# Performance work log

Hardware: AMD Instinct MI355X
Metric: run time of the kernel (lower is better)

Reference implementation:

```python
import jax, jax.numpy as jnp
import numpy as np
from jax import lax

B, C, H, W = 2, 128, 128, 128
Hs, Ws = 64, 64
DG, KK = 8, 9          # deformable groups, kernel positions (3x3)
CG = C // DG           # channels per deformable group = 16
COUT = C // 2          # dcn output channels = 64


def setup_inputs() -> dict:
    key = jax.random.key(0)
    ks = jax.random.split(key, 9)
    s = 0.05
    return {
        "feat_l": jax.random.normal(ks[0], (B, C, H, W), jnp.float32),
        "feat_s": jax.random.normal(ks[1], (B, C, Hs, Ws), jnp.float32),
        "fsm_w": jax.random.normal(ks[2], (C, C, 1, 1), jnp.float32) * s,
        "offset_w": jax.random.normal(ks[3], (C, 2 * C, 1, 1), jnp.float32) * s,
        "com_w": jax.random.normal(ks[4], (3 * DG * KK, C, 3, 3), jnp.float32) * s,
        "com_b": jax.random.normal(ks[5], (3 * DG * KK,), jnp.float32) * s,
        "dcn_w": jax.random.normal(ks[6], (COUT, C, 3, 3), jnp.float32) * s,
        "dcn_b": jax.random.normal(ks[7], (COUT,), jnp.float32) * s,
        "cat_w": jax.random.normal(ks[8], (C, COUT, 1, 1), jnp.float32) * s,
    }


def _conv(x, w, pad):
    return lax.conv_general_dilated(x, w, (1, 1), [(pad, pad), (pad, pad)],
                                    dimension_numbers=("NCHW", "OIHW", "NCHW"))


def _bilinear(feat_g, py, px):
    # feat_g: [B,DG,CG,H,W]; py/px: [B,DG,KK,H,W] fractional sample coords.
    Hf, Wf = feat_g.shape[-2], feat_g.shape[-1]
    y0 = jnp.floor(py)
    x0 = jnp.floor(px)
    ly = py - y0
    lx = px - x0
    y0i = y0.astype(jnp.int32)
    x0i = x0.astype(jnp.int32)
    flat = feat_g.reshape(B, DG, 1, CG, Hf * Wf)  # broadcast over KK

    def gather(yi, xi, wgt):
        valid = ((yi >= 0) & (yi < Hf) & (xi >= 0) & (xi < Wf)).astype(feat_g.dtype)
        idx = (jnp.clip(yi, 0, Hf - 1) * Wf + jnp.clip(xi, 0, Wf - 1))
        idx = idx.reshape(B, DG, KK, 1, H * W)
        v = jnp.take_along_axis(flat, idx, axis=-1)  # [B,DG,KK,CG,H*W]
        return v * (wgt * valid).reshape(B, DG, KK, 1, H * W)

    acc = (gather(y0i, x0i, (1 - ly) * (1 - lx))
           + gather(y0i, x0i + 1, (1 - ly) * lx)
           + gather(y0i + 1, x0i, ly * (1 - lx))
           + gather(y0i + 1, x0i + 1, ly * lx))
    return acc.reshape(B, DG, KK, CG, H, W)


def reference(feat_l, feat_s, fsm_w, offset_w, com_w, com_b, dcn_w, dcn_b, cat_w):
    # nearest-neighbor upsample of feat_s to feat_l's HxW (F.interpolate nearest)
    idx_h = (jnp.arange(H) * Hs) // H
    idx_w = (jnp.arange(W) * Ws) // W
    feat_up = feat_s[:, :, idx_h][:, :, :, idx_w]

    feat_arm = jax.nn.relu(_conv(feat_l, fsm_w, 0))                       # FSM (1x1 conv+relu)
    off_feat = jax.nn.relu(_conv(jnp.concatenate([feat_arm, feat_up * 2], axis=1), offset_w, 0))

    # DCNv2 pack: 3x3 conv -> (o1, o2, mask)
    om = _conv(off_feat, com_w, 1) + com_b[None, :, None, None]
    o1, o2, m = jnp.split(om, 3, axis=1)
    offset = jnp.concatenate([o1, o2], axis=1).reshape(B, DG, KK, 2, H, W)  # (y,x) per (g,pos)
    mask = jax.nn.sigmoid(m).reshape(B, DG, KK, H, W)

    # sampling coords: p + kernel offset + learned offset (stride=1, pad=1, dil=1)
    kyy = (jnp.arange(KK) // 3 - 1).astype(jnp.float32)
    kxx = (jnp.arange(KK) % 3 - 1).astype(jnp.float32)
    py = (jnp.arange(H, dtype=jnp.float32)[None, None, None, :, None]
          + kyy[None, None, :, None, None] + offset[:, :, :, 0])
    px = (jnp.arange(W, dtype=jnp.float32)[None, None, None, None, :]
          + kxx[None, None, :, None, None] + offset[:, :, :, 1])

    feat_g = feat_up.reshape(B, DG, CG, H, W)
    val = _bilinear(feat_g, py, px) * mask[:, :, :, None]  # [B,DG,KK,CG,H,W]

    w_r = dcn_w.reshape(COUT, DG, CG, KK)
    out = jnp.einsum('bgkchw,ogck->bohw', val, w_r) + dcn_b[None, :, None, None]
    feat_align = jax.nn.relu(out)

    return jax.nn.relu(_conv(feat_align, cat_w, 0)) + feat_arm
```

## Files before the change

### kernel.cpp

```cpp
#include <hip/hip_runtime.h>
#include <cstdint>
#include <cstddef>


typedef _Float16 f16x8 __attribute__((ext_vector_type(8)));
typedef _Float16 f16x4 __attribute__((ext_vector_type(4)));
typedef float    f32x4 __attribute__((ext_vector_type(4)));

__device__ __forceinline__ float relu_(float x) { return fmaxf(x, 0.f); }

template<int MODE, int CIN>
__global__ __launch_bounds__(256) void conv1x1_kernel(
    const float* __restrict__ in1, const float* __restrict__ in2,
    const float* __restrict__ Wm, float* __restrict__ out)
{
  constexpr int IN1C = (MODE == 2) ? 64 : 128;
  const int b  = blockIdx.y;
  const int p0 = blockIdx.x * 64;
  const int tid = threadIdx.x;
  const int tx = tid & 7;
  const int ty = tid >> 3;

  __shared__ float Xs[16][64];
  __shared__ float Wt[16][128];

  float acc[4][8];
#pragma unroll
  for (int i = 0; i < 4; ++i)
#pragma unroll
    for (int j = 0; j < 8; ++j) acc[i][j] = 0.f;

  const int cS  = tid >> 4;
  const int pxS = (tid & 15) * 4;
  const int ocS = (tid & 15) * 8;

  for (int cc = 0; cc < CIN; cc += 16) {
    __syncthreads();
    {
      int gc = cc + cS;
      float4 v;
      if (MODE == 1 && gc >= 128) {
        int sc = gc - 128;
        float t[4];
#pragma unroll
        for (int j = 0; j < 4; ++j) {
          int pp = p0 + pxS + j;
          int hh = pp >> 7, ww = pp & 127;
          t[j] = 2.f * in2[((size_t)(b * 128 + sc) << 12) + ((hh >> 1) << 6) + (ww >> 1)];
        }
        v = make_float4(t[0], t[1], t[2], t[3]);
      } else {
        v = *(const float4*)(in1 + ((size_t)(b * IN1C + gc) << 14) + p0 + pxS);
      }
      *(float4*)&Xs[cS][pxS] = v;
#pragma unroll
      for (int j = 0; j < 8; ++j)
        Wt[cS][ocS + j] = Wm[(ocS + j) * CIN + cc + cS];
    }
    __syncthreads();
#pragma unroll
    for (int c = 0; c < 16; ++c) {
      float4 wv = *(const float4*)&Wt[c][ty * 4];
      float4 x0 = *(const float4*)&Xs[c][tx * 8];
      float4 x1 = *(const float4*)&Xs[c][tx * 8 + 4];
      float xs[8] = {x0.x, x0.y, x0.z, x0.w, x1.x, x1.y, x1.z, x1.w};
      float wf[4] = {wv.x, wv.y, wv.z, wv.w};
#pragma unroll
      for (int i = 0; i < 4; ++i)
#pragma unroll
        for (int j = 0; j < 8; ++j)
          acc[i][j] = fmaf(wf[i], xs[j], acc[i][j]);
    }
  }

#pragma unroll
  for (int i = 0; i < 4; ++i) {
    int oc = ty * 4 + i;
    size_t base = ((size_t)(b * 128 + oc) << 14) + p0 + tx * 8;
    float r[8];
#pragma unroll
    for (int j = 0; j < 8; ++j) r[j] = relu_(acc[i][j]);
    if (MODE == 2) {
#pragma unroll
      for (int j = 0; j < 8; ++j) r[j] += in2[base + j];
    }
    *(float4*)(out + base)     = make_float4(r[0], r[1], r[2], r[3]);
    *(float4*)(out + base + 4) = make_float4(r[4], r[5], r[6], r[7]);
  }
}

__global__ __launch_bounds__(256) void t2h2_kernel(
    const float* __restrict__ fl, const float* __restrict__ fs,
    _Float16* __restrict__ flTh, _Float16* __restrict__ fsTh)
{
  const int bx = blockIdx.x;
  const float* src;
  _Float16* dst;
  int HW, p0;
  if (bx < 512) { src = fl; dst = flTh; HW = 16384; p0 = bx * 32; }
  else          { src = fs; dst = fsTh; HW = 4096;  p0 = (bx - 512) * 32; }
  const int b  = blockIdx.z;
  const int c0 = blockIdx.y * 32;
  const int tid = threadIdx.x;
  __shared__ float T[32][33];
  {
    int pxl = tid & 31, cy = tid >> 5;
#pragma unroll
    for (int j = 0; j < 4; ++j) {
      int c = cy + j * 8;
      T[c][pxl] = src[((size_t)(b * 128 + c0 + c)) * HW + p0 + pxl];
    }
  }
  __syncthreads();
  {
    int cq = tid & 7, pr = tid >> 3;
    f16x4 v;
#pragma unroll
    for (int e = 0; e < 4; ++e) v[e] = (_Float16)T[cq * 4 + e][pr];
    *(f16x4*)&dst[(((size_t)b * HW) + p0 + pr) * 128 + c0 + cq * 4] = v;
  }
}

__global__ __launch_bounds__(256) void wfall_kernel(
    const float* __restrict__ fsm_w, const float* __restrict__ offset_w,
    const float* __restrict__ com_w, const float* __restrict__ dcn_w,
    const float* __restrict__ cat_w,
    _Float16* __restrict__ WfA, _Float16* __restrict__ WfB,
    _Float16* __restrict__ WfP, _Float16* __restrict__ Wf2,
    _Float16* __restrict__ WfC)
{
  const int bid = blockIdx.x;
  if (bid < 8) {
    int idx = bid * 256 + threadIdx.x;
    int lane = idx & 63;
    int t = idx >> 6;
    int m = t & 7, q = t >> 3;
    int oc = m * 16 + (lane & 15);
    int c0 = q * 32 + (lane >> 4) * 8;
    f16x8 v;
#pragma unroll
    for (int j = 0; j < 8; ++j) v[j] = (_Float16)fsm_w[oc * 128 + c0 + j];
    ((f16x8*)WfA)[idx] = v;
  } else if (bid < 24) {
    int idx = (bid - 8) * 256 + threadIdx.x;
    int lane = idx & 63;
    int t = idx >> 6;
    int m = t & 7, q = t >> 3;
    int oc = m * 16 + (lane & 15);
    int c0 = q * 32 + (lane >> 4) * 8;
    float s = (q >= 4) ? 2.f : 1.f;
    f16x8 v;
#pragma unroll
    for (int j = 0; j < 8; ++j) v[j] = (_Float16)(offset_w[oc * 256 + c0 + j] * s);
    ((f16x8*)WfB)[idx] = v;
  } else if (bid < 168) {
    int idx = (bid - 24) * 256 + threadIdx.x;
    int lane = idx & 63;
    int t = idx >> 6;
    int m = t & 7;
    int t2 = t >> 3;
    int half = t2 & 1, q = t2 >> 1;
    int kk = q >> 2;
    int ic0 = (q & 3) * 32 + (lane >> 4) * 8;
    int oc = half * 128 + m * 16 + (lane & 15);
    f16x8 v;
#pragma unroll
    for (int j = 0; j < 8; ++j) {
      float x = (oc < 216) ? com_w[((size_t)oc * 128 + ic0 + j) * 9 + kk] : 0.f;
      v[j] = (_Float16)x;
    }
    ((f16x8*)WfP)[idx] = v;
  } else if (bid < 204) {
    int idx = (bid - 168) * 256 + threadIdx.x;
    int lane = idx & 63;
    int t = idx >> 6;
    int m = t & 3, q = t >> 2;
    int oc = m * 16 + (lane & 15);
    f16x8 v;
#pragma unroll
    for (int j = 0; j < 8; ++j) {
      int rp = q * 32 + (lane >> 4) * 8 + j;
      int c = rp & 15, tt = rp >> 4;
      int g = tt / 9, k = tt % 9;
      v[j] = (_Float16)dcn_w[((size_t)oc * 128 + g * 16 + c) * 9 + k];
    }
    ((f16x8*)Wf2)[idx] = v;
  } else {
    int idx = (bid - 204) * 256 + threadIdx.x;
    int lane = idx & 63;
    int t = idx >> 6;
    int m = t & 7, q = t >> 3;
    int oc = m * 16 + (lane & 15);
    int k0 = q * 32 + (lane >> 4) * 8;
    f16x8 v;
#pragma unroll
    for (int j = 0; j < 8; ++j) v[j] = (_Float16)cat_w[oc * 64 + k0 + j];
    ((f16x8*)WfC)[idx] = v;
  }
}

__global__ __launch_bounds__(256) void fsm_gemm_kernel(
    const _Float16* __restrict__ flTh, const _Float16* __restrict__ WfA,
    float* __restrict__ arm, _Float16* __restrict__ armh)
{
  const int b    = blockIdx.y;
  const int tid  = threadIdx.x;
  const int wv   = tid >> 6;
  const int lane = tid & 63;
  const int px0  = blockIdx.x * 64 + wv * 16;
  const int pxl  = px0 + (lane & 15);

  f32x4 acc[8];
#pragma unroll
  for (int m = 0; m < 8; ++m) acc[m] = (f32x4){0.f, 0.f, 0.f, 0.f};

  const f16x8* Bp = (const f16x8*)flTh + (((size_t)b << 14) + pxl) * 16 + (lane >> 4);
  const f16x8* Ap = (const f16x8*)WfA + lane;

#pragma unroll
  for (int q = 0; q < 4; ++q) {
    f16x8 bf = Bp[q * 4];
#pragma unroll
    for (int m = 0; m < 8; ++m)
      acc[m] = __builtin_amdgcn_mfma_f32_16x16x32_f16(Ap[(q * 8 + m) * 64], bf, acc[m], 0, 0, 0);
  }

  const int r0 = (lane >> 4) * 4;
#pragma unroll
  for (int m = 0; m < 8; ++m) {
    f16x4 h;
#pragma unroll
    for (int r = 0; r < 4; ++r) {
      float v = relu_(acc[m][r]);
      arm[((size_t)(b * 128 + m * 16 + r0 + r) << 14) + pxl] = v;
      h[r] = (_Float16)v;
    }
    *(f16x4*)&armh[(((size_t)b << 14) + pxl) * 128 + m * 16 + r0] = h;
  }
}

__global__ __launch_bounds__(256) void off_gemm_kernel(
    const _Float16* __restrict__ armh, const _Float16* __restrict__ fsTh,
    const _Float16* __restrict__ WfB, _Float16* __restrict__ offh)
{
  const int b    = blockIdx.y;
  const int tid  = threadIdx.x;
  const int wv   = tid >> 6;
  const int lane = tid & 63;
  const int px0  = blockIdx.x * 64 + wv * 16;
  const int pxl  = px0 + (lane & 15);
  const int h = pxl >> 7, w = pxl & 127;
  const int pup = ((h >> 1) << 6) + (w >> 1);

  f32x4 acc[8];
#pragma unroll
  for (int m = 0; m < 8; ++m) acc[m] = (f32x4){0.f, 0.f, 0.f, 0.f};

  const f16x8* BpA = (const f16x8*)armh + (((size_t)b << 14) + pxl) * 16 + (lane >> 4);
  const f16x8* BpU = (const f16x8*)fsTh + (((size_t)b << 12) + pup) * 16 + (lane >> 4);
  const f16x8* Ap  = (const f16x8*)WfB + lane;

#pragma unroll
  for (int q = 0; q < 8; ++q) {
    f16x8 bf = (q < 4) ? BpA[q * 4] : BpU[(q - 4) * 4];
#pragma unroll
    for (int m = 0; m < 8; ++m)
      acc[m] = __builtin_amdgcn_mfma_f32_16x16x32_f16(Ap[(q * 8 + m) * 64], bf, acc[m], 0, 0, 0);
  }

  const int r0 = (lane >> 4) * 4;
#pragma unroll
  for (int m = 0; m < 8; ++m) {
    f16x4 hh;
#pragma unroll
    for (int r = 0; r < 4; ++r) hh[r] = (_Float16)relu_(acc[m][r]);
    *(f16x4*)&offh[(((size_t)b << 14) + pxl) * 128 + m * 16 + r0] = hh;
  }
}

__global__ __launch_bounds__(256) void com_gemm_kernel(
    const _Float16* __restrict__ offh, const _Float16* __restrict__ WfP,
    const float* __restrict__ cb, _Float16* __restrict__ omh)
{
  const int b    = blockIdx.z;
  const int half = blockIdx.y;
  const int tid  = threadIdx.x;
  const int lane = tid & 63;
  const int px0  = blockIdx.x * 64 + (tid >> 6) * 16;
  const int pxl  = px0 + (lane & 15);
  const int h = pxl >> 7, w = pxl & 127;

  __shared__ f16x8 As[512];

  f32x4 acc[8];
#pragma unroll
  for (int m = 0; m < 8; ++m) acc[m] = (f32x4){0.f, 0.f, 0.f, 0.f};

  const f16x8* Bbase = (const f16x8*)offh + ((size_t)b << 14) * 16 + (lane >> 4);
  const f16x8* Wp    = (const f16x8*)WfP + half * 512 + tid * 2;
  const f16x8 zero = {(_Float16)0.f, (_Float16)0.f, (_Float16)0.f, (_Float16)0.f,
                      (_Float16)0.f, (_Float16)0.f, (_Float16)0.f, (_Float16)0.f};

  auto loadB = [&](int t) -> f16x8 {
    const int kk = t >> 2, ic4 = t & 3;
    const int hh = h + kk / 3 - 1;
    const int ww = w + kk % 3 - 1;
    const bool valid = ((unsigned)hh < 128u) && ((unsigned)ww < 128u);
    const int ps = valid ? ((hh << 7) + ww) : 0;
    f16x8 bf = Bbase[(size_t)ps * 16 + ic4 * 4];
    return valid ? bf : zero;
  };

  f16x8 rA0 = Wp[0], rA1 = Wp[1];
  f16x8 bfA = loadB(0), bfB = loadB(1);

#pragma unroll 1
  for (int tt = 0; tt < 18; ++tt) {
    const int t0 = tt * 2;
    __syncthreads();
    As[tid * 2] = rA0; As[tid * 2 + 1] = rA1;
    __syncthreads();
    rA0 = Wp[(t0 + 1) * 1024]; rA1 = Wp[(t0 + 1) * 1024 + 1];
    {
      f16x8 bu = bfA;
      if (t0 + 2 < 36) bfA = loadB(t0 + 2);
#pragma unroll
      for (int m = 0; m < 8; ++m)
        acc[m] = __builtin_amdgcn_mfma_f32_16x16x32_f16(As[m * 64 + lane], bu, acc[m], 0, 0, 0);
    }
    __syncthreads();
    As[tid * 2] = rA0; As[tid * 2 + 1] = rA1;
    __syncthreads();
    if (t0 + 2 < 36) { rA0 = Wp[(t0 + 2) * 1024]; rA1 = Wp[(t0 + 2) * 1024 + 1]; }
    {
      f16x8 bu = bfB;
      if (t0 + 3 < 36) bfB = loadB(t0 + 3);
#pragma unroll
      for (int m = 0; m < 8; ++m)
        acc[m] = __builtin_amdgcn_mfma_f32_16x16x32_f16(As[m * 64 + lane], bu, acc[m], 0, 0, 0);
    }
  }

  const int r0i = (lane >> 4) * 4;
#pragma unroll
  for (int m = 0; m < 8; ++m) {
#pragma unroll
    for (int r = 0; r < 4; ++r) {
      int oc = half * 128 + m * 16 + r0i + r;
      if (oc < 216)
        omh[((size_t)(b * 216 + oc) << 14) + pxl] = (_Float16)(acc[m][r] + cb[oc]);
    }
  }
}

__global__ __launch_bounds__(256) void dcn_fused_kernel(
    const _Float16* __restrict__ fsTh, const _Float16* __restrict__ omh,
    const _Float16* __restrict__ Wf2, const float* __restrict__ db,
    _Float16* __restrict__ alh)
{
  const int b    = blockIdx.y;
  const int tid  = threadIdx.x;
  const int wv   = tid >> 6;
  const int lane = tid & 63;
  const int px0  = blockIdx.x * 64 + wv * 16;
  const int pxl  = px0 + (lane & 15);
  const int h = pxl >> 7, w = pxl & 127;
  const int t9add = lane >> 5;
  const int chalf = ((lane >> 4) & 1) << 3;

  const _Float16* omp = omh + (((size_t)b * 216) << 14) + pxl;
  const _Float16* fb = fsTh + ((size_t)b << 19);
  const f16x8* Ap = (const f16x8*)Wf2 + lane;

  f32x4 acc[4];
#pragma unroll
  for (int m = 0; m < 4; ++m) acc[m] = (f32x4){0.f, 0.f, 0.f, 0.f};

#pragma unroll 1
  for (int q = 0; q < 36; ++q) {
    const int t9 = 2 * q + t9add;
    const int g = t9 / 9;
    const int k = t9 - g * 9;

    const float offy = (float)omp[(size_t)(g * 18 + 2 * k) << 14];
    const float offx = (float)omp[(size_t)(g * 18 + 2 * k + 1) << 14];
    const float mraw = (float)omp[(size_t)(144 + t9) << 14];
    const float mv = 1.f / (1.f + __expf(-mraw));

    const float py  = (float)(h + k / 3 - 1) + offy;
    const float pxx = (float)(w + k % 3 - 1) + offx;
    const float y0f = floorf(py), x0f = floorf(pxx);
    const float ly = py - y0f, lx = pxx - x0f;
    const int y0 = (int)y0f, x0i = (int)x0f;
    const int y1 = y0 + 1, x1 = x0i + 1;

    const int y0c = min(max(y0, 0), 127), y1c = min(max(y1, 0), 127);
    const int x0c = min(max(x0i, 0), 127), x1c = min(max(x1, 0), 127);

    float w00 = (1.f - ly) * (1.f - lx) * mv;
    float w01 = (1.f - ly) * lx * mv;
    float w10 = ly * (1.f - lx) * mv;
    float w11 = ly * lx * mv;
    const bool vy0 = (unsigned)y0 < 128u, vy1 = (unsigned)y1 < 128u;
    const bool vx0 = (unsigned)x0i < 128u, vx1 = (unsigned)x1 < 128u;
    w00 = (vy0 && vx0) ? w00 : 0.f;
    w01 = (vy0 && vx1) ? w01 : 0.f;
    w10 = (vy1 && vx0) ? w10 : 0.f;
    w11 = (vy1 && vx1) ? w11 : 0.f;

    const int gb = g * 16 + chalf;
    const int a00 = ((((y0c >> 1) << 6) + (x0c >> 1)) << 7) + gb;
    const int a01 = ((((y0c >> 1) << 6) + (x1c >> 1)) << 7) + gb;
    const int a10 = ((((y1c >> 1) << 6) + (x0c >> 1)) << 7) + gb;
    const int a11 = ((((y1c >> 1) << 6) + (x1c >> 1)) << 7) + gb;

    f16x8 t00 = *(const f16x8*)(fb + a00);
    f16x8 t01 = *(const f16x8*)(fb + a01);
    f16x8 t10 = *(const f16x8*)(fb + a10);
    f16x8 t11 = *(const f16x8*)(fb + a11);

    f16x8 bf;
#pragma unroll
    for (int j = 0; j < 8; ++j)
      bf[j] = (_Float16)(w00 * (float)t00[j] + w01 * (float)t01[j]
                       + w10 * (float)t10[j] + w11 * (float)t11[j]);

    const f16x8* ap = Ap + q * 256;
#pragma unroll
    for (int m = 0; m < 4; ++m)
      acc[m] = __builtin_amdgcn_mfma_f32_16x16x32_f16(ap[m * 64], bf, acc[m], 0, 0, 0);
  }

  const int r0 = (lane >> 4) * 4;
#pragma unroll
  for (int m = 0; m < 4; ++m) {
    f16x4 hv;
#pragma unroll
    for (int r = 0; r < 4; ++r) {
      int oc = m * 16 + r0 + r;
      hv[r] = (_Float16)relu_(acc[m][r] + db[oc]);
    }
    *(f16x4*)&alh[(((size_t)b << 14) + pxl) * 64 + m * 16 + r0] = hv;
  }
}

__global__ __launch_bounds__(256) void cat_gemm_kernel(
    const _Float16* __restrict__ alh, const _Float16* __restrict__ WfC,
    const float* __restrict__ arm, float* __restrict__ out)
{
  const int b    = blockIdx.y;
  const int tid  = threadIdx.x;
  const int wv   = tid >> 6;
  const int lane = tid & 63;
  const int px0  = blockIdx.x * 64 + wv * 16;
  const int pxl  = px0 + (lane & 15);

  f32x4 acc[8];
#pragma unroll
  for (int m = 0; m < 8; ++m) acc[m] = (f32x4){0.f, 0.f, 0.f, 0.f};

  const f16x8* Bp = (const f16x8*)alh + (((size_t)b << 14) + pxl) * 8 + (lane >> 4);
  const f16x8* Ap = (const f16x8*)WfC + lane;

#pragma unroll
  for (int q = 0; q < 2; ++q) {
    f16x8 bf = Bp[q * 4];
#pragma unroll
    for (int m = 0; m < 8; ++m)
      acc[m] = __builtin_amdgcn_mfma_f32_16x16x32_f16(Ap[(q * 8 + m) * 64], bf, acc[m], 0, 0, 0);
  }

  const int r0 = (lane >> 4) * 4;
#pragma unroll
  for (int m = 0; m < 8; ++m) {
#pragma unroll
    for (int r = 0; r < 4; ++r) {
      int oc = m * 16 + r0 + r;
      size_t a = ((size_t)(b * 128 + oc) << 14) + pxl;
      out[a] = relu_(acc[m][r]) + arm[a];
    }
  }
}

__global__ __launch_bounds__(256) void com_conv_kernel(
    const float* __restrict__ x, const float* __restrict__ cw,
    const float* __restrict__ cb, float* __restrict__ om)
{
  const int b    = blockIdx.z;
  const int ocg  = blockIdx.y;
  const int tile = blockIdx.x;
  const int th = (tile >> 2) * 32, tw = (tile & 3) * 32;
  const int tid = threadIdx.x;
  const int lw = (tid & 7) * 4;
  const int lh = tid >> 3;

  __shared__ float Xs[8 * 34 * 34];

  float acc[8][4];
#pragma unroll
  for (int a = 0; a < 8; ++a)
#pragma unroll
    for (int p = 0; p < 4; ++p) acc[a][p] = 0.f;

  for (int cc = 0; cc < 128; cc += 8) {
    __syncthreads();
    for (int idx = tid; idx < 8 * 1156; idx += 256) {
      int ic  = idx / 1156;
      int rem = idx - ic * 1156;
      int yy  = rem / 34;
      int xx  = rem - yy * 34;
      int gh = th + yy - 1, gw = tw + xx - 1;
      float v = 0.f;
      if ((unsigned)gh < 128u && (unsigned)gw < 128u)
        v = x[((size_t)(b * 128 + cc + ic) << 14) + (gh << 7) + gw];
      Xs[idx] = v;
    }
    __syncthreads();
#pragma unroll 1
    for (int ic = 0; ic < 8; ++ic) {
      float xr[3][6];
#pragma unroll
      for (int ky = 0; ky < 3; ++ky)
#pragma unroll
        for (int xx = 0; xx < 6; ++xx)
          xr[ky][xx] = Xs[ic * 1156 + (lh + ky) * 34 + lw + xx];
      const float* wp = cw + ((size_t)(ocg * 8) * 128 + (cc + ic)) * 9;
#pragma unroll
      for (int a = 0; a < 8; ++a) {
        const float* w9 = wp + a * 1152;
#pragma unroll
        for (int ky = 0; ky < 3; ++ky)
#pragma unroll
          for (int kx = 0; kx < 3; ++kx) {
            float wv = w9[ky * 3 + kx];
#pragma unroll
            for (int p = 0; p < 4; ++p)
              acc[a][p] = fmaf(wv, xr[ky][kx + p], acc[a][p]);
          }
      }
    }
  }

#pragma unroll
  for (int a = 0; a < 8; ++a) {
    int oc = ocg * 8 + a;
    float bv = cb[oc];
    float4 r = make_float4(acc[a][0] + bv, acc[a][1] + bv,
                           acc[a][2] + bv, acc[a][3] + bv);
    *(float4*)(om + ((size_t)(b * 216 + oc) << 14) + ((th + lh) << 7) + tw + lw) = r;
  }
}

__global__ __launch_bounds__(256) void wt_kernel(const float* __restrict__ dw,
                                                 float* __restrict__ wT)
{
  int idx = blockIdx.x * 256 + threadIdx.x;
  int o    = idx & 63;
  int rest = idx >> 6;
  int k    = rest % 9;
  int gc   = rest / 9;
  wT[idx] = dw[(o * 128 + gc) * 9 + k];
}

__global__ __launch_bounds__(256) void dcn_kernel(
    const float* __restrict__ fs, const float* __restrict__ om,
    const float* __restrict__ wT, const float* __restrict__ db,
    float* __restrict__ al)
{
  const int b   = blockIdx.y;
  const int p0  = blockIdx.x * 32;
  const int tid = threadIdx.x;
  const int px  = tid & 31;
  const int g   = tid >> 5;
  const int p = p0 + px;
  const int h = p >> 7, w = p & 127;

  float acc[64];
#pragma unroll
  for (int o = 0; o < 64; ++o) acc[o] = 0.f;

  const size_t omb = ((size_t)b * 216) << 14;
  const float* fsg = fs + (((size_t)(b * 128 + g * 16)) << 12);
  const float* wg  = wT + g * (16 * 9 * 64);

#pragma unroll 1
  for (int k = 0; k < 9; ++k) {
    float offy = om[omb + ((size_t)(g * 18 + 2 * k) << 14) + p];
    float offx = om[omb + ((size_t)(g * 18 + 2 * k + 1) << 14) + p];
    float mraw = om[omb + ((size_t)(144 + g * 9 + k) << 14) + p];
    float mv = 1.f / (1.f + __expf(-mraw));

    float py  = (float)(h + k / 3 - 1) + offy;
    float pxx = (float)(w + k % 3 - 1) + offx;
    float y0f = floorf(py), x0f = floorf(pxx);
    float ly = py - y0f, lx = pxx - x0f;
    int y0 = (int)y0f, x0i = (int)x0f;
    int y1 = y0 + 1, x1 = x0i + 1;

    int y0c = min(max(y0, 0), 127), y1c = min(max(y1, 0), 127);
    int x0c = min(max(x0i, 0), 127), x1c = min(max(x1, 0), 127);
    int ry0 = (y0c >> 1) << 6, ry1 = (y1c >> 1) << 6;
    int cx0 = x0c >> 1, cx1 = x1c >> 1;

    float w00 = (1.f - ly) * (1.f - lx) * mv;
    float w01 = (1.f - ly) * lx * mv;
    float w10 = ly * (1.f - lx) * mv;
    float w11 = ly * lx * mv;
    bool vy0 = (unsigned)y0 < 128u, vy1 = (unsigned)y1 < 128u;
    bool vx0 = (unsigned)x0i < 128u, vx1 = (unsigned)x1 < 128u;
    w00 = (vy0 && vx0) ? w00 : 0.f;
    w01 = (vy0 && vx1) ? w01 : 0.f;
    w10 = (vy1 && vx0) ? w10 : 0.f;
    w11 = (vy1 && vx1) ? w11 : 0.f;

#pragma unroll 1
    for (int c = 0; c < 16; ++c) {
      const float* fc = fsg + (c << 12);
      float v00 = fc[ry0 + cx0];
      float v01 = fc[ry0 + cx1];
      float v10 = fc[ry1 + cx0];
      float v11 = fc[ry1 + cx1];
      float v = w00 * v00 + w01 * v01 + w10 * v10 + w11 * v11;
      const float* wp = wg + (c * 9 + k) * 64;
#pragma unroll
      for (int oq = 0; oq < 16; ++oq) {
        float4 w4 = *(const float4*)(wp + oq * 4);
        acc[oq * 4 + 0] = fmaf(v, w4.x, acc[oq * 4 + 0]);
        acc[oq * 4 + 1] = fmaf(v, w4.y, acc[oq * 4 + 1]);
        acc[oq * 4 + 2] = fmaf(v, w4.z, acc[oq * 4 + 2]);
        acc[oq * 4 + 3] = fmaf(v, w4.w, acc[oq * 4 + 3]);
      }
    }
  }

  __shared__ float red[256][17];
  const int px2 = tid & 31;
  const int og  = tid >> 5;
#pragma unroll
  for (int r = 0; r < 4; ++r) {
    __syncthreads();
#pragma unroll
    for (int j = 0; j < 16; ++j) red[tid][j] = acc[r * 16 + j];
    __syncthreads();
#pragma unroll
    for (int jj = 0; jj < 2; ++jj) {
      int ol = og * 2 + jj;
      float s = 0.f;
#pragma unroll
      for (int gg = 0; gg < 8; ++gg) s += red[gg * 32 + px2][ol];
      int oc = r * 16 + ol;
      s += db[oc];
      al[((size_t)(b * 64 + oc) << 14) + p0 + px2] = fmaxf(s, 0.f);
    }
  }
}

extern "C" void kernel_launch(void* const* d_in, const int* in_sizes, int n_in,
                              void* d_out, int out_size, void* d_ws, size_t ws_size,
                              hipStream_t stream)
{
  const float* feat_l   = (const float*)d_in[0];
  const float* feat_s   = (const float*)d_in[1];
  const float* fsm_w    = (const float*)d_in[2];
  const float* offset_w = (const float*)d_in[3];
  const float* com_w    = (const float*)d_in[4];
  const float* com_b    = (const float*)d_in[5];
  const float* dcn_w    = (const float*)d_in[6];
  const float* dcn_b    = (const float*)d_in[7];
  const float* cat_w    = (const float*)d_in[8];
  float* out = (float*)d_out;
  float* ws  = (float*)d_ws;

  const size_t NEED = (size_t)(4194304 + 7077888 + 2097152 + 1048576 + 37748736) * 4;

  if (ws_size >= NEED) {
    float* arm      = ws;
    _Float16* omh   = (_Float16*)(ws + 4194304);
    _Float16* alh   = (_Float16*)(ws + 11272192);
    _Float16* Wf2   = (_Float16*)(ws + 12320768);
    _Float16* WfC   = (_Float16*)(ws + 12357632);
    _Float16* fsTh  = (_Float16*)(ws + 13369344);
    _Float16* flTh  = (_Float16*)(ws + 13893632);
    _Float16* armh  = (_Float16*)(ws + 15990784);
    _Float16* offh  = (_Float16*)(ws + 18087936);
    _Float16* WfA   = (_Float16*)(ws + 39059456);
    _Float16* WfB   = (_Float16*)(ws + 39067648);
    _Float16* WfP   = (_Float16*)(ws + 39084032);

    hipLaunchKernelGGL(wfall_kernel, dim3(208), dim3(256), 0, stream,
                       fsm_w, offset_w, com_w, dcn_w, cat_w, WfA, WfB, WfP, Wf2, WfC);
    hipLaunchKernelGGL(t2h2_kernel, dim3(640, 4, 2), dim3(256), 0, stream,
                       feat_l, feat_s, flTh, fsTh);
    hipLaunchKernelGGL(fsm_gemm_kernel, dim3(256, 2), dim3(256), 0, stream,
                       flTh, WfA, arm, armh);
    hipLaunchKernelGGL(off_gemm_kernel, dim3(256, 2), dim3(256), 0, stream,
                       armh, fsTh, WfB, offh);
    hipLaunchKernelGGL(com_gemm_kernel, dim3(256, 2, 2), dim3(256), 0, stream,
                       offh, WfP, com_b, omh);
    hipLaunchKernelGGL(dcn_fused_kernel, dim3(256, 2), dim3(256), 0, stream,
                       fsTh, omh, Wf2, dcn_b, alh);
    hipLaunchKernelGGL(cat_gemm_kernel, dim3(256, 2), dim3(256), 0, stream,
                       alh, WfC, arm, out);
  } else {
    float* arm = ws;
    float* off = ws + 4194304;
    float* om  = ws + 8388608;
    float* al  = ws + 15466496;
    float* wT  = ws + 17563648;

    hipLaunchKernelGGL(wt_kernel, dim3(288), dim3(256), 0, stream, dcn_w, wT);
    hipLaunchKernelGGL((conv1x1_kernel<0, 128>), dim3(256, 2), dim3(256), 0, stream,
                       feat_l, nullptr, fsm_w, arm);
    hipLaunchKernelGGL((conv1x1_kernel<1, 256>), dim3(256, 2), dim3(256), 0, stream,
                       arm, feat_s, offset_w, off);
    hipLaunchKernelGGL(com_conv_kernel, dim3(16, 27, 2), dim3(256), 0, stream,
                       off, com_w, com_b, om);
    hipLaunchKernelGGL(dcn_kernel, dim3(512, 2), dim3(256), 0, stream,
                       feat_s, om, wT, dcn_b, al);
    hipLaunchKernelGGL((conv1x1_kernel<2, 64>), dim3(256, 2), dim3(256), 0, stream,
                       al, arm, cat_w, out);
  }
}
```

Before: 186.6 us.

## Use group-major feat_s layout for DCN gathers and deepen prefetch in com/dcn kernels

The transpose kernel now also writes feat_s in a per-deformable-group layout (16 channels contiguous per pixel within each group plane). The DCN kernel gathers its bilinear corner samples from this layout, so the samples taken by one group sit closer together in memory. The DCN loop now handles two kernel-position pairs per iteration and prefetches the next offset and mask values, overlapping those loads with the sampling and MFMA work. The com GEMM stages two K-steps of weights into a doubled shared buffer per barrier pair, which halves the number of synchronisations. In exchange this adds an extra fp16 copy of feat_s, more workspace, and higher register pressure.

```diff
diff --git a/kernel.cpp b/kernel.cpp
--- a/kernel.cpp
+++ b/kernel.cpp
@@ -91,7 +91,8 @@
 
 __global__ __launch_bounds__(256) void t2h2_kernel(
     const float* __restrict__ fl, const float* __restrict__ fs,
-    _Float16* __restrict__ flTh, _Float16* __restrict__ fsTh)
+    _Float16* __restrict__ flTh, _Float16* __restrict__ fsTh,
+    _Float16* __restrict__ fsThg)
 {
   const int bx = blockIdx.x;
   const float* src;
@@ -118,6 +119,11 @@
 #pragma unroll
     for (int e = 0; e < 4; ++e) v[e] = (_Float16)T[cq * 4 + e][pr];
     *(f16x4*)&dst[(((size_t)b * HW) + p0 + pr) * 128 + c0 + cq * 4] = v;
+    if (bx >= 512) {
+      int c = c0 + cq * 4;
+      int g = c >> 4, co = c & 15;
+      *(f16x4*)&fsThg[((((size_t)(b * 8 + g)) << 12) + p0 + pr) * 16 + co] = v;
+    }
   }
 }
 
@@ -290,7 +296,7 @@
   const int pxl  = px0 + (lane & 15);
   const int h = pxl >> 7, w = pxl & 127;
 
-  __shared__ f16x8 As[512];
+  __shared__ f16x8 As[1024];
 
   f32x4 acc[8];
 #pragma unroll
@@ -311,34 +317,29 @@
     return valid ? bf : zero;
   };
 
-  f16x8 rA0 = Wp[0], rA1 = Wp[1];
-  f16x8 bfA = loadB(0), bfB = loadB(1);
+  f16x8 rA0 = Wp[0], rA1 = Wp[1], rA2 = Wp[1024], rA3 = Wp[1024 + 1];
+  f16x8 bf0 = loadB(0), bf1 = loadB(1);
 
 #pragma unroll 1
-  for (int tt = 0; tt < 18; ++tt) {
-    const int t0 = tt * 2;
+  for (int s = 0; s < 18; ++s) {
     __syncthreads();
-    As[tid * 2] = rA0; As[tid * 2 + 1] = rA1;
+    As[tid * 2]           = rA0;
+    As[tid * 2 + 1]       = rA1;
+    As[512 + tid * 2]     = rA2;
+    As[512 + tid * 2 + 1] = rA3;
     __syncthreads();
-    rA0 = Wp[(t0 + 1) * 1024]; rA1 = Wp[(t0 + 1) * 1024 + 1];
-    {
-      f16x8 bu = bfA;
-      if (t0 + 2 < 36) bfA = loadB(t0 + 2);
-#pragma unroll
-      for (int m = 0; m < 8; ++m)
-        acc[m] = __builtin_amdgcn_mfma_f32_16x16x32_f16(As[m * 64 + lane], bu, acc[m], 0, 0, 0);
-    }
-    __syncthreads();
-    As[tid * 2] = rA0; As[tid * 2 + 1] = rA1;
-    __syncthreads();
-    if (t0 + 2 < 36) { rA0 = Wp[(t0 + 2) * 1024]; rA1 = Wp[(t0 + 2) * 1024 + 1]; }
-    {
-      f16x8 bu = bfB;
-      if (t0 + 3 < 36) bfB = loadB(t0 + 3);
-#pragma unroll
-      for (int m = 0; m < 8; ++m)
-        acc[m] = __builtin_amdgcn_mfma_f32_16x16x32_f16(As[m * 64 + lane], bu, acc[m], 0, 0, 0);
-    }
+    if (s < 17) {
+      rA0 = Wp[(2 * s + 2) * 1024];     rA1 = Wp[(2 * s + 2) * 1024 + 1];
+      rA2 = Wp[(2 * s + 3) * 1024];     rA3 = Wp[(2 * s + 3) * 1024 + 1];
+    }
+    f16x8 buA = bf0, buB = bf1;
+    if (s < 17) { bf0 = loadB(2 * s + 2); bf1 = loadB(2 * s + 3); }
+#pragma unroll
+    for (int m = 0; m < 8; ++m)
+      acc[m] = __builtin_amdgcn_mfma_f32_16x16x32_f16(As[m * 64 + lane], buA, acc[m], 0, 0, 0);
+#pragma unroll
+    for (int m = 0; m < 8; ++m)
+      acc[m] = __builtin_amdgcn_mfma_f32_16x16x32_f16(As[512 + m * 64 + lane], buB, acc[m], 0, 0, 0);
   }
 
   const int r0i = (lane >> 4) * 4;
@@ -354,7 +355,7 @@
 }
 
 __global__ __launch_bounds__(256) void dcn_fused_kernel(
-    const _Float16* __restrict__ fsTh, const _Float16* __restrict__ omh,
+    const _Float16* __restrict__ fsThg, const _Float16* __restrict__ omh,
     const _Float16* __restrict__ Wf2, const float* __restrict__ db,
     _Float16* __restrict__ alh)
 {
@@ -369,66 +370,108 @@
   const int chalf = ((lane >> 4) & 1) << 3;
 
   const _Float16* omp = omh + (((size_t)b * 216) << 14) + pxl;
-  const _Float16* fb = fsTh + ((size_t)b << 19);
+  const _Float16* fb = fsThg + ((size_t)b << 19);
   const f16x8* Ap = (const f16x8*)Wf2 + lane;
 
   f32x4 acc[4];
 #pragma unroll
   for (int m = 0; m < 4; ++m) acc[m] = (f32x4){0.f, 0.f, 0.f, 0.f};
 
-#pragma unroll 1
-  for (int q = 0; q < 36; ++q) {
+  auto loadOm = [&](int q, float& oy, float& ox, float& mr) {
     const int t9 = 2 * q + t9add;
     const int g = t9 / 9;
     const int k = t9 - g * 9;
-
-    const float offy = (float)omp[(size_t)(g * 18 + 2 * k) << 14];
-    const float offx = (float)omp[(size_t)(g * 18 + 2 * k + 1) << 14];
-    const float mraw = (float)omp[(size_t)(144 + t9) << 14];
-    const float mv = 1.f / (1.f + __expf(-mraw));
-
-    const float py  = (float)(h + k / 3 - 1) + offy;
-    const float pxx = (float)(w + k % 3 - 1) + offx;
+    oy = (float)omp[(size_t)(g * 18 + 2 * k) << 14];
+    ox = (float)omp[(size_t)(g * 18 + 2 * k + 1) << 14];
+    mr = (float)omp[(size_t)(144 + t9) << 14];
+  };
+
+  auto coords = [&](int q, float oy, float ox, float mr,
+                    float& w00, float& w01, float& w10, float& w11,
+                    int& a00, int& a01, int& a10, int& a11) {
+    const int t9 = 2 * q + t9add;
+    const int g = t9 / 9;
+    const int k = t9 - g * 9;
+    const float mv = 1.f / (1.f + __expf(-mr));
+    const float py  = (float)(h + k / 3 - 1) + oy;
+    const float pxx = (float)(w + k % 3 - 1) + ox;
     const float y0f = floorf(py), x0f = floorf(pxx);
     const float ly = py - y0f, lx = pxx - x0f;
     const int y0 = (int)y0f, x0i = (int)x0f;
     const int y1 = y0 + 1, x1 = x0i + 1;
-
     const int y0c = min(max(y0, 0), 127), y1c = min(max(y1, 0), 127);
     const int x0c = min(max(x0i, 0), 127), x1c = min(max(x1, 0), 127);
-
-    float w00 = (1.f - ly) * (1.f - lx) * mv;
-    float w01 = (1.f - ly) * lx * mv;
-    float w10 = ly * (1.f - lx) * mv;
-    float w11 = ly * lx * mv;
+    w00 = (1.f - ly) * (1.f - lx) * mv;
+    w01 = (1.f - ly) * lx * mv;
+    w10 = ly * (1.f - lx) * mv;
+    w11 = ly * lx * mv;
     const bool vy0 = (unsigned)y0 < 128u, vy1 = (unsigned)y1 < 128u;
     const bool vx0 = (unsigned)x0i < 128u, vx1 = (unsigned)x1 < 128u;
     w00 = (vy0 && vx0) ? w00 : 0.f;
     w01 = (vy0 && vx1) ? w01 : 0.f;
     w10 = (vy1 && vx0) ? w10 : 0.f;
     w11 = (vy1 && vx1) ? w11 : 0.f;
-
-    const int gb = g * 16 + chalf;
-    const int a00 = ((((y0c >> 1) << 6) + (x0c >> 1)) << 7) + gb;
-    const int a01 = ((((y0c >> 1) << 6) + (x1c >> 1)) << 7) + gb;
-    const int a10 = ((((y1c >> 1) << 6) + (x0c >> 1)) << 7) + gb;
-    const int a11 = ((((y1c >> 1) << 6) + (x1c >> 1)) << 7) + gb;
-
-    f16x8 t00 = *(const f16x8*)(fb + a00);
-    f16x8 t01 = *(const f16x8*)(fb + a01);
-    f16x8 t10 = *(const f16x8*)(fb + a10);
-    f16x8 t11 = *(const f16x8*)(fb + a11);
-
-    f16x8 bf;
+    const int gb = (g << 16) + chalf;
+    a00 = gb + ((y0c >> 1) << 10) + ((x0c >> 1) << 4);
+    a01 = gb + ((y0c >> 1) << 10) + ((x1c >> 1) << 4);
+    a10 = gb + ((y1c >> 1) << 10) + ((x0c >> 1) << 4);
+    a11 = gb + ((y1c >> 1) << 10) + ((x1c >> 1) << 4);
+  };
+
+  float oyA, oxA, mrA, oyB, oxB, mrB;
+  loadOm(0, oyA, oxA, mrA);
+  loadOm(1, oyB, oxB, mrB);
+
+#pragma unroll 1
+  for (int qq = 0; qq < 18; ++qq) {
+    const int qA = 2 * qq, qB = 2 * qq + 1;
+
+    float wA00, wA01, wA10, wA11; int aA00, aA01, aA10, aA11;
+    coords(qA, oyA, oxA, mrA, wA00, wA01, wA10, wA11, aA00, aA01, aA10, aA11);
+    f16x8 tA00 = *(const f16x8*)(fb + aA00);
+    f16x8 tA01 = *(const f16x8*)(fb + aA01);
+    f16x8 tA10 = *(const f16x8*)(fb + aA10);
+    f16x8 tA11 = *(const f16x8*)(fb + aA11);
+
+    float wB00, wB01, wB10, wB11; int aB00, aB01, aB10, aB11;
+    coords(qB, oyB, oxB, mrB, wB00, wB01, wB10, wB11, aB00, aB01, aB10, aB11);
+    f16x8 tB00 = *(const f16x8*)(fb + aB00);
+    f16x8 tB01 = *(const f16x8*)(fb + aB01);
+    f16x8 tB10 = *(const f16x8*)(fb + aB10);
+    f16x8 tB11 = *(const f16x8*)(fb + aB11);
+
+    float noyA = 0.f, noxA = 0.f, nmrA = 0.f, noyB = 0.f, noxB = 0.f, nmrB = 0.f;
+    if (qq < 17) {
+      loadOm(qA + 2, noyA, noxA, nmrA);
+      loadOm(qB + 2, noyB, noxB, nmrB);
+    }
+
+    f16x8 bfA;
 #pragma unroll
     for (int j = 0; j < 8; ++j)
-      bf[j] = (_Float16)(w00 * (float)t00[j] + w01 * (float)t01[j]
-                       + w10 * (float)t10[j] + w11 * (float)t11[j]);
-
-    const f16x8* ap = Ap + q * 256;
-#pragma unroll
-    for (int m = 0; m < 4; ++m)
-      acc[m] = __builtin_amdgcn_mfma_f32_16x16x32_f16(ap[m * 64], bf, acc[m], 0, 0, 0);
+      bfA[j] = (_Float16)(wA00 * (float)tA00[j] + wA01 * (float)tA01[j]
+                        + wA10 * (float)tA10[j] + wA11 * (float)tA11[j]);
+    {
+      const f16x8* ap = Ap + qA * 256;
+#pragma unroll
+      for (int m = 0; m < 4; ++m)
+        acc[m] = __builtin_amdgcn_mfma_f32_16x16x32_f16(ap[m * 64], bfA, acc[m], 0, 0, 0);
+    }
+
+    f16x8 bfB;
+#pragma unroll
+    for (int j = 0; j < 8; ++j)
+      bfB[j] = (_Float16)(wB00 * (float)tB00[j] + wB01 * (float)tB01[j]
+                        + wB10 * (float)tB10[j] + wB11 * (float)tB11[j]);
+    {
+      const f16x8* ap = Ap + qB * 256;
+#pragma unroll
+      for (int m = 0; m < 4; ++m)
+        acc[m] = __builtin_amdgcn_mfma_f32_16x16x32_f16(ap[m * 64], bfB, acc[m], 0, 0, 0);
+    }
+
+    oyA = noyA; oxA = noxA; mrA = nmrA;
+    oyB = noyB; oxB = noxB; mrB = nmrB;
   }
 
   const int r0 = (lane >> 4) * 4;
@@ -686,11 +729,12 @@
     _Float16* WfA   = (_Float16*)(ws + 39059456);
     _Float16* WfB   = (_Float16*)(ws + 39067648);
     _Float16* WfP   = (_Float16*)(ws + 39084032);
+    _Float16* fsThg = (_Float16*)(ws + 39231488);
 
     hipLaunchKernelGGL(wfall_kernel, dim3(208), dim3(256), 0, stream,
                        fsm_w, offset_w, com_w, dcn_w, cat_w, WfA, WfB, WfP, Wf2, WfC);
     hipLaunchKernelGGL(t2h2_kernel, dim3(640, 4, 2), dim3(256), 0, stream,
-                       feat_l, feat_s, flTh, fsTh);
+                       feat_l, feat_s, flTh, fsTh, fsThg);
     hipLaunchKernelGGL(fsm_gemm_kernel, dim3(256, 2), dim3(256), 0, stream,
                        flTh, WfA, arm, armh);
     hipLaunchKernelGGL(off_gemm_kernel, dim3(256, 2), dim3(256), 0, stream,
@@ -698,7 +742,7 @@
     hipLaunchKernelGGL(com_gemm_kernel, dim3(256, 2, 2), dim3(256), 0, stream,
                        offh, WfP, com_b, omh);
     hipLaunchKernelGGL(dcn_fused_kernel, dim3(256, 2), dim3(256), 0, stream,
-                       fsTh, omh, Wf2, dcn_b, alh);
+                       fsThg, omh, Wf2, dcn_b, alh);
     hipLaunchKernelGGL(cat_gemm_kernel, dim3(256, 2), dim3(256), 0, stream,
                        alh, WfC, arm, out);
   } else {
```

Measured after the change: 191.3 us. 1.02x slower.

## Stage group-major feat_s tile in LDS for deformable bilinear gathers

Applied to the files above, without the earlier changes.

The transpose kernel now also writes a group-major fp16 copy of feat_s, with 16 channels per group stored contiguously. Each DCN block cooperatively loads a 5x36 half-resolution tile for all 8 groups into shared memory. The four bilinear corner fetches then read from LDS, falling back to global memory only when an offset lands outside the tile. This replaces scattered global/L2 gathers with LDS reads, at the cost of a ~46KB LDS footprint per block (lower occupancy), an upfront tile load and an extra workspace buffer.

```diff
diff --git a/kernel.cpp b/kernel.cpp
--- a/kernel.cpp
+++ b/kernel.cpp
@@ -91,7 +91,8 @@
 
 __global__ __launch_bounds__(256) void t2h2_kernel(
     const float* __restrict__ fl, const float* __restrict__ fs,
-    _Float16* __restrict__ flTh, _Float16* __restrict__ fsTh)
+    _Float16* __restrict__ flTh, _Float16* __restrict__ fsTh,
+    _Float16* __restrict__ fsThg)
 {
   const int bx = blockIdx.x;
   const float* src;
@@ -118,6 +119,11 @@
 #pragma unroll
     for (int e = 0; e < 4; ++e) v[e] = (_Float16)T[cq * 4 + e][pr];
     *(f16x4*)&dst[(((size_t)b * HW) + p0 + pr) * 128 + c0 + cq * 4] = v;
+    if (bx >= 512) {
+      int c = c0 + cq * 4;
+      int g = c >> 4, co = c & 15;
+      *(f16x4*)&fsThg[((((size_t)(b * 8 + g)) << 12) + p0 + pr) * 16 + co] = v;
+    }
   }
 }
 
@@ -354,7 +360,7 @@
 }
 
 __global__ __launch_bounds__(256) void dcn_fused_kernel(
-    const _Float16* __restrict__ fsTh, const _Float16* __restrict__ omh,
+    const _Float16* __restrict__ fsThg, const _Float16* __restrict__ omh,
     const _Float16* __restrict__ Wf2, const float* __restrict__ db,
     _Float16* __restrict__ alh)
 {
@@ -368,8 +374,27 @@
   const int t9add = lane >> 5;
   const int chalf = ((lane >> 4) & 1) << 3;
 
+  const int hb  = blockIdx.x >> 1;
+  const int w0  = (blockIdx.x & 1) << 6;
+  const int ty0 = min(max((hb - 4) >> 1, 0), 59);
+  const int tx0 = (w0 == 0) ? 0 : 28;
+
+  __shared__ _Float16 Xs[8 * 5 * 36 * 16];
+
+  {
+    const _Float16* src0 = fsThg + ((size_t)b << 19);
+    for (int v = tid; v < 2880; v += 256) {
+      int row = v / 72;
+      int col = v - row * 72;
+      int g = row / 5, dy = row - g * 5;
+      const _Float16* s = src0 + ((size_t)((g << 12) + (ty0 + dy) * 64 + tx0) << 4) + col * 8;
+      *(f16x8*)&Xs[row * (36 * 16) + col * 8] = *(const f16x8*)s;
+    }
+  }
+  __syncthreads();
+
   const _Float16* omp = omh + (((size_t)b * 216) << 14) + pxl;
-  const _Float16* fb = fsTh + ((size_t)b << 19);
+  const _Float16* fb  = fsThg + ((size_t)b << 19);
   const f16x8* Ap = (const f16x8*)Wf2 + lane;
 
   f32x4 acc[4];
@@ -408,16 +433,28 @@
     w10 = (vy1 && vx0) ? w10 : 0.f;
     w11 = (vy1 && vx1) ? w11 : 0.f;
 
-    const int gb = g * 16 + chalf;
-    const int a00 = ((((y0c >> 1) << 6) + (x0c >> 1)) << 7) + gb;
-    const int a01 = ((((y0c >> 1) << 6) + (x1c >> 1)) << 7) + gb;
-    const int a10 = ((((y1c >> 1) << 6) + (x0c >> 1)) << 7) + gb;
-    const int a11 = ((((y1c >> 1) << 6) + (x1c >> 1)) << 7) + gb;
-
-    f16x8 t00 = *(const f16x8*)(fb + a00);
-    f16x8 t01 = *(const f16x8*)(fb + a01);
-    f16x8 t10 = *(const f16x8*)(fb + a10);
-    f16x8 t11 = *(const f16x8*)(fb + a11);
+    const int ta = y0c >> 1, tb = y1c >> 1, tc = x0c >> 1, td = x1c >> 1;
+    const int dy0 = ta - ty0, dy1 = tb - ty0, dx0 = tc - tx0, dx1 = td - tx0;
+    const bool ib00 = ((unsigned)dy0 < 5u) & ((unsigned)dx0 < 36u);
+    const bool ib01 = ((unsigned)dy0 < 5u) & ((unsigned)dx1 < 36u);
+    const bool ib10 = ((unsigned)dy1 < 5u) & ((unsigned)dx0 < 36u);
+    const bool ib11 = ((unsigned)dy1 < 5u) & ((unsigned)dx1 < 36u);
+
+    const int gb5 = g * 5;
+    const int cy0 = min(max(dy0, 0), 4), cy1 = min(max(dy1, 0), 4);
+    const int cx0 = min(max(dx0, 0), 35), cx1 = min(max(dx1, 0), 35);
+    f16x8 t00 = *(const f16x8*)&Xs[((gb5 + cy0) * 36 + cx0) * 16 + chalf];
+    f16x8 t01 = *(const f16x8*)&Xs[((gb5 + cy0) * 36 + cx1) * 16 + chalf];
+    f16x8 t10 = *(const f16x8*)&Xs[((gb5 + cy1) * 36 + cx0) * 16 + chalf];
+    f16x8 t11 = *(const f16x8*)&Xs[((gb5 + cy1) * 36 + cx1) * 16 + chalf];
+
+    if (!(ib00 & ib01 & ib10 & ib11)) {
+      const _Float16* fg = fb + ((size_t)g << 16) + chalf;
+      if (!ib00) t00 = *(const f16x8*)(fg + (((ta << 6) + tc) << 4));
+      if (!ib01) t01 = *(const f16x8*)(fg + (((ta << 6) + td) << 4));
+      if (!ib10) t10 = *(const f16x8*)(fg + (((tb << 6) + tc) << 4));
+      if (!ib11) t11 = *(const f16x8*)(fg + (((tb << 6) + td) << 4));
+    }
 
     f16x8 bf;
 #pragma unroll
@@ -686,11 +723,12 @@
     _Float16* WfA   = (_Float16*)(ws + 39059456);
     _Float16* WfB   = (_Float16*)(ws + 39067648);
     _Float16* WfP   = (_Float16*)(ws + 39084032);
+    _Float16* fsThg = (_Float16*)(ws + 39231488);
 
     hipLaunchKernelGGL(wfall_kernel, dim3(208), dim3(256), 0, stream,
                        fsm_w, offset_w, com_w, dcn_w, cat_w, WfA, WfB, WfP, Wf2, WfC);
     hipLaunchKernelGGL(t2h2_kernel, dim3(640, 4, 2), dim3(256), 0, stream,
-                       feat_l, feat_s, flTh, fsTh);
+                       feat_l, feat_s, flTh, fsTh, fsThg);
     hipLaunchKernelGGL(fsm_gemm_kernel, dim3(256, 2), dim3(256), 0, stream,
                        flTh, WfA, arm, armh);
     hipLaunchKernelGGL(off_gemm_kernel, dim3(256, 2), dim3(256), 0, stream,
@@ -698,7 +736,7 @@
     hipLaunchKernelGGL(com_gemm_kernel, dim3(256, 2, 2), dim3(256), 0, stream,
                        offh, WfP, com_b, omh);
     hipLaunchKernelGGL(dcn_fused_kernel, dim3(256, 2), dim3(256), 0, stream,
-                       fsTh, omh, Wf2, dcn_b, alh);
+                       fsThg, omh, Wf2, dcn_b, alh);
     hipLaunchKernelGGL(cat_gemm_kernel, dim3(256, 2), dim3(256), 0, stream,
                        alh, WfC, arm, out);
   } else {
```

Result: no change. 187.3 us (+0.4%).
